# Optimization experiments

Measured on AMD Instinct MI355X. Metric: run time of the kernel, lower is better.

Reference implementation:

```python
import jax, jax.numpy as jnp
from jax import lax
import numpy as np

# Constants matching module config
DT = 0.0005            # integrator dt (phys_model default)
SPF = 10               # simulation substeps per output frame
GRAVITY = jnp.array([0.0, 0.0, -9.81], dtype=jnp.float32)
MASS_EPS = 0.1         # keep masses strictly positive

# ---- quaternion helpers (xyzw, matching warp layout: transform = [pos(3), quat(4)]) ----

def quat_mul(a, b):
    ax, ay, az, aw = a[..., 0], a[..., 1], a[..., 2], a[..., 3]
    bx, by, bz, bw = b[..., 0], b[..., 1], b[..., 2], b[..., 3]
    return jnp.stack([
        aw * bx + ax * bw + ay * bz - az * by,
        aw * by - ax * bz + ay * bw + az * bx,
        aw * bz + ax * by - ay * bx + az * bw,
        aw * bw - ax * bx - ay * by - az * bz,
    ], -1)


def quat_rotate(q, v):
    qv, qw = q[..., :3], q[..., 3:4]
    t = 2.0 * jnp.cross(qv, v)
    return v + qw * t + jnp.cross(qv, t)


def quat_from_axis_angle(axis, theta):
    # axis: (3,), theta: (bs,) -> (bs,4)
    half = 0.5 * theta
    return jnp.concatenate([axis[None, :] * jnp.sin(half)[:, None],
                            jnp.cos(half)[:, None]], -1)


def normalize(v, axis=-1):
    return v / jnp.linalg.norm(v, axis=axis, keepdims=True).clip(1e-8)


# ---- forward kinematics along the articulated chain (eval_fk) ----

def eval_fk(root_p, root_q, root_w, root_v, jq, jqd, axes, offsets):
    """root_*: (bs,...); jq,jqd: (bs,B); axes,offsets: (B,3).
    Returns body_q (bs,B+1,7), body_qd (bs,B+1,6) [angular,linear]."""
    def step(carry, inp):
        p, q, w, v = carry
        theta, thetad, axis, off = inp
        off_w = quat_rotate(q, off)                   # (bs,3)
        p_c = p + off_w
        q_c = quat_mul(q, quat_from_axis_angle(axis, theta))
        axis_w = quat_rotate(q, axis)
        w_c = w + axis_w * thetad[:, None]
        v_c = v + jnp.cross(w, off_w)
        carry = (p_c, q_c, w_c, v_c)
        return carry, carry
    inps = (jq.T, jqd.T, axes, offsets)               # leading dim B
    _, (ps, qs, ws, vs) = lax.scan(step, (root_p, root_q, root_w, root_v), inps)
    body_p = jnp.concatenate([root_p[None], ps], 0)   # (B+1,bs,3)
    body_r = jnp.concatenate([root_q[None], qs], 0)
    body_w = jnp.concatenate([root_w[None], ws], 0)
    body_v = jnp.concatenate([root_v[None], vs], 0)
    body_q = jnp.concatenate([body_p, body_r], -1).transpose(1, 0, 2)   # (bs,B+1,7)
    body_qd = jnp.concatenate([body_w, body_v], -1).transpose(1, 0, 2)  # (bs,B+1,6)
    return body_q, body_qd


def reference(q_init, qd_init, torques, res_f, refs, target_ke, target_kd,
              body_mass, joint_axes, joint_offsets):
    bs, ndof = q_init.shape
    B = ndof - 7
    axes = normalize(joint_axes)                      # (B,3)
    mass = body_mass + MASS_EPS                       # (bs,B+1)

    # initial maximal-coordinate state from generalized coords
    root_p = q_init[:, 0:3]
    root_q = normalize(q_init[:, 3:7])
    root_w = qd_init[:, 0:3]
    root_v = qd_init[:, 3:6]
    jq = q_init[:, 7:]
    jqd = qd_init[:, 6:]

    def sim_step(state, u):
        p, q, w, v, jq, jqd = state
        tau, ref, rf = u                              # (bs,6+B),(bs,6+B),(bs,B+1,6)
        m0 = mass[:, 0:1]
        # free root body: residual wrench + act wrench + gravity, semi-implicit Euler
        v = v + DT * ((tau[:, 3:6] + rf[:, 0, 3:6]) / m0 + GRAVITY)
        w = w + DT * (tau[:, 0:3] + rf[:, 0, 0:3]) / m0
        p = p + DT * v
        wq = jnp.concatenate([w, jnp.zeros_like(w[:, :1])], -1)
        q = normalize(q + DT * 0.5 * quat_mul(wq, q))
        # revolute joints: PD target (ke,kd) + actuation + residual torque on axis
        rf_tau = jnp.einsum('nbd,bd->nb', rf[:, 1:, 0:3], axes)   # (bs,B)
        tau_j = tau[:, 6:] + target_ke * (ref[:, 6:] - jq) - target_kd * jqd + rf_tau
        jqd = jqd + DT * tau_j / mass[:, 1:]
        jq = jq + DT * jqd
        return (p, q, w, v, jq, jqd), None

    def frame_step(state, u_frame):
        state, _ = lax.scan(sim_step, state, u_frame)
        p, q, w, v, jq, jqd = state
        bq, bqd = eval_fk(p, q, w, v, jq, jqd, axes, joint_offsets)
        return state, (bq, bqd)

    nsteps = torques.shape[0]
    F = nsteps // SPF                                 # output frames after frame 0
    u = (torques.reshape(F, SPF, bs, -1),
         refs.reshape(F, SPF, bs, -1),
         res_f.reshape(F, SPF, bs, B + 1, 6))

    state0 = (root_p, root_q, root_w, root_v, jq, jqd)
    bq0, bqd0 = eval_fk(*state0, axes, joint_offsets)  # frame 0 = init FK
    _, (bqs, bqds) = lax.scan(frame_step, state0, u)
    wp_pos = jnp.concatenate([bq0[None], bqs], 0)      # (T,bs,B+1,7)
    wp_vel = jnp.concatenate([bqd0[None], bqds], 0)    # (T,bs,B+1,6)
    return wp_pos, wp_vel


def setup_inputs() -> dict:
    key = jax.random.key(0)
    ks = jax.random.split(key, 10)
    bs, B, S = 1024, 25, 150
    return {
        'q_init': jax.random.normal(ks[0], (bs, 7 + B), jnp.float32),
        'qd_init': 0.1 * jax.random.normal(ks[1], (bs, 6 + B), jnp.float32),
        'torques': jax.random.normal(ks[2], (S, bs, 6 + B), jnp.float32),
        'res_f': jax.random.normal(ks[3], (S, bs, B + 1, 6), jnp.float32),
        'refs': jax.random.normal(ks[4], (S, bs, 6 + B), jnp.float32),
        'target_ke': jax.random.uniform(ks[5], (bs, B), jnp.float32),
        'target_kd': jax.random.uniform(ks[6], (bs, B), jnp.float32),
        'body_mass': jax.random.uniform(ks[7], (bs, B + 1), jnp.float32),
        'joint_axes': jax.random.normal(ks[8], (B, 3), jnp.float32),
        'joint_offsets': 0.2 * jax.random.normal(ks[9], (B, 3), jnp.float32),
    }
```

## Files before the change

### kernel.cpp

```cpp
#include <hip/hip_runtime.h>

#define DT     0.0005f
#define NENV   1024
#define NB     25
#define SPF    10
#define NFRM   16
#define SNAP_STRIDE 64

#define JTHREADS (NENV*NB)
#define JBLOCKS  (JTHREADS/64)
#define RBLOCKS  (NENV/64)
#define TQ_SLAB  (NENV*31)
#define RF_SLAB  (NENV*156)

__global__ __launch_bounds__(64) void integrate_kernel(
    const float* __restrict__ q_init,
    const float* __restrict__ qd_init,
    const float* __restrict__ torques,
    const float* __restrict__ res_f,
    const float* __restrict__ refs,
    const float* __restrict__ target_ke,
    const float* __restrict__ target_kd,
    const float* __restrict__ body_mass,
    const float* __restrict__ joint_axes,
    float* __restrict__ snap)
{
    const int bid = (int)blockIdx.x;

    if (bid < JBLOCKS) {
        const int t   = bid*64 + (int)threadIdx.x;
        const int env = t / NB;
        const int j   = t - env*NB;

        float a0 = joint_axes[j*3+0];
        float a1 = joint_axes[j*3+1];
        float a2 = joint_axes[j*3+2];
        float rn = 1.0f / fmaxf(sqrtf(a0*a0 + a1*a1 + a2*a2), 1e-8f);
        const float ax = a0*rn, ay = a1*rn, az = a2*rn;
        const float ke   = target_ke[env*NB + j];
        const float kd   = target_kd[env*NB + j];
        const float invm = 1.0f / (body_mass[env*(NB+1) + 1 + j] + 0.1f);
        float jq  = q_init [env*32 + 7 + j];
        float jqd = qd_init[env*31 + 6 + j];

        const int tq_off = env*31  + 6 + j;
        const int rf_off = env*156 + 6 + 6*j;

        snap[(size_t)env*SNAP_STRIDE + 13 + j] = jq;
        snap[(size_t)env*SNAP_STRIDE + 38 + j] = jqd;

        #pragma unroll 1
        for (int f = 1; f < NFRM; ++f) {
            float ta[SPF], rr[SPF], r0[SPF], r1[SPF], r2[SPF];
            #pragma unroll
            for (int k = 0; k < SPF; ++k) {
                const int s = (f-1)*SPF + k;
                ta[k] = torques[(size_t)s*TQ_SLAB + tq_off];
                rr[k] = refs   [(size_t)s*TQ_SLAB + tq_off];
                const float* rf = res_f + (size_t)s*RF_SLAB + rf_off;
                float2 ab = *(const float2*)rf;
                r0[k] = ab.x; r1[k] = ab.y; r2[k] = rf[2];
            }
            #pragma unroll
            for (int k = 0; k < SPF; ++k) {
                float rftau = r0[k]*ax + r1[k]*ay + r2[k]*az;
                float tj = ta[k] + ke*(rr[k] - jq) - kd*jqd + rftau;
                jqd += DT * tj * invm;
                jq  += DT * jqd;
            }
            float* sp = snap + ((size_t)f*NENV + env) * SNAP_STRIDE;
            sp[13 + j] = jq;
            sp[38 + j] = jqd;
        }
    } else {
        const int env = (bid - JBLOCKS)*64 + (int)threadIdx.x;

        float px = q_init[env*32+0], py = q_init[env*32+1], pz = q_init[env*32+2];
        float q0 = q_init[env*32+3], q1 = q_init[env*32+4];
        float q2 = q_init[env*32+5], q3 = q_init[env*32+6];
        float rn = 1.0f / fmaxf(sqrtf(q0*q0 + q1*q1 + q2*q2 + q3*q3), 1e-8f);
        float qx = q0*rn, qy = q1*rn, qz = q2*rn, qw = q3*rn;
        float wx = qd_init[env*31+0], wy = qd_init[env*31+1], wz = qd_init[env*31+2];
        float vx = qd_init[env*31+3], vy = qd_init[env*31+4], vz = qd_init[env*31+5];
        const float invm0 = 1.0f / (body_mass[env*(NB+1)] + 0.1f);

        {
            float* sp = snap + (size_t)env * SNAP_STRIDE;
            sp[0]=px; sp[1]=py; sp[2]=pz;
            sp[3]=qx; sp[4]=qy; sp[5]=qz; sp[6]=qw;
            sp[7]=wx; sp[8]=wy; sp[9]=wz;
            sp[10]=vx; sp[11]=vy; sp[12]=vz;
        }

        #pragma unroll 1
        for (int f = 1; f < NFRM; ++f) {
            float  tb[SPF][6];
            float4 ra[SPF];
            float2 rb[SPF];
            #pragma unroll
            for (int k = 0; k < SPF; ++k) {
                const int s = (f-1)*SPF + k;
                const float* tq = torques + (size_t)s*TQ_SLAB + env*31;
                tb[k][0]=tq[0]; tb[k][1]=tq[1]; tb[k][2]=tq[2];
                tb[k][3]=tq[3]; tb[k][4]=tq[4]; tb[k][5]=tq[5];
                const float* rf = res_f + (size_t)s*RF_SLAB + env*156;
                ra[k] = *(const float4*)rf;
                rb[k] = *(const float2*)(rf + 4);
            }
            #pragma unroll
            for (int k = 0; k < SPF; ++k) {
                vx += DT * ((tb[k][3] + rb[k].x) * invm0);
                vy += DT * ((tb[k][4] + rb[k].y) * invm0);
                vz += DT * ((tb[k][5] + ra[k].w) * invm0 - 9.81f);
                wx += DT * (tb[k][0] + ra[k].x) * invm0;
                wy += DT * (tb[k][1] + ra[k].y) * invm0;
                wz += DT * (tb[k][2] + ra[k].z) * invm0;
                px += DT * vx; py += DT * vy; pz += DT * vz;
                float dqx =  wx*qw + wy*qz - wz*qy;
                float dqy = -wx*qz + wy*qw + wz*qx;
                float dqz =  wx*qy - wy*qx + wz*qw;
                float dqw = -(wx*qx + wy*qy + wz*qz);
                float nqx = qx + 0.5f*DT*dqx;
                float nqy = qy + 0.5f*DT*dqy;
                float nqz = qz + 0.5f*DT*dqz;
                float nqw = qw + 0.5f*DT*dqw;
                float nrm = sqrtf(nqx*nqx + nqy*nqy + nqz*nqz + nqw*nqw);
                float rq  = 1.0f / fmaxf(nrm, 1e-8f);
                qx = nqx*rq; qy = nqy*rq; qz = nqz*rq; qw = nqw*rq;
            }
            float* sp = snap + ((size_t)f*NENV + env) * SNAP_STRIDE;
            sp[0]=px; sp[1]=py; sp[2]=pz;
            sp[3]=qx; sp[4]=qy; sp[5]=qz; sp[6]=qw;
            sp[7]=wx; sp[8]=wy; sp[9]=wz;
            sp[10]=vx; sp[11]=vy; sp[12]=vz;
        }
    }
}

__global__ __launch_bounds__(64) void integrate_kernel_fixed(
    const float* __restrict__ q_init,
    const float* __restrict__ qd_init,
    const float* __restrict__ torques,
    const float* __restrict__ res_f,
    const float* __restrict__ refs,
    const float* __restrict__ target_ke,
    const float* __restrict__ target_kd,
    const float* __restrict__ body_mass,
    const float* __restrict__ joint_axes,
    float* __restrict__ snap)
{
    const int bid = (int)blockIdx.x;

    if (bid < JBLOCKS) {
        const int t   = bid*64 + (int)threadIdx.x;
        const int env = t / NB;
        const int j   = t - env*NB;

        float a0 = joint_axes[j*3+0];
        float a1 = joint_axes[j*3+1];
        float a2 = joint_axes[j*3+2];
        float rn = 1.0f / fmaxf(sqrtf(a0*a0 + a1*a1 + a2*a2), 1e-8f);
        const float ax = a0*rn, ay = a1*rn, az = a2*rn;
        const float ke   = target_ke[env*NB + j];
        const float kd   = target_kd[env*NB + j];
        const float invm = 1.0f / (body_mass[env*(NB+1) + 1 + j] + 0.1f);
        float jq  = q_init [env*32 + 7 + j];
        float jqd = qd_init[env*31 + 6 + j];

        const int tq_off = env*31  + 6 + j;
        const int rf_off = env*156 + 6 + 6*j;

        snap[(size_t)env*SNAP_STRIDE + 13 + j] = jq;
        snap[(size_t)env*SNAP_STRIDE + 38 + j] = jqd;

        #pragma unroll 1
        for (int f = 1; f < NFRM; ++f) {
            float ta[SPF], rr[SPF], r0[SPF], r1[SPF], r2[SPF];
            #pragma unroll
            for (int k = 0; k < SPF; ++k) {
                const int s = (f-1)*SPF + k;
                ta[k] = torques[(size_t)s*TQ_SLAB + tq_off];
                rr[k] = refs   [(size_t)s*TQ_SLAB + tq_off];
                const float* rf = res_f + (size_t)s*RF_SLAB + rf_off;
                float2 ab = *(const float2*)rf;
                r0[k] = ab.x; r1[k] = ab.y; r2[k] = rf[2];
            }
            #pragma unroll
            for (int k = 0; k < SPF; ++k) {
                float rftau = r0[k]*ax + r1[k]*ay + r2[k]*az;
                float tj = ta[k] + ke*(rr[k] - jq) - kd*jqd + rftau;
                jqd += DT * tj * invm;
                jq  += DT * jqd;
            }
            float* sp = snap + ((size_t)f*NENV + env) * SNAP_STRIDE;
            sp[13 + j] = jq;
            sp[38 + j] = jqd;
        }
    } else {
        const int env = (bid - JBLOCKS)*64 + (int)threadIdx.x;

        float px = q_init[env*32+0], py = q_init[env*32+1], pz = q_init[env*32+2];
        float q0 = q_init[env*32+3], q1 = q_init[env*32+4];
        float q2 = q_init[env*32+5], q3 = q_init[env*32+6];
        float rn = 1.0f / fmaxf(sqrtf(q0*q0 + q1*q1 + q2*q2 + q3*q3), 1e-8f);
        float qx = q0*rn, qy = q1*rn, qz = q2*rn, qw = q3*rn;
        float wx = qd_init[env*31+0], wy = qd_init[env*31+1], wz = qd_init[env*31+2];
        float vx = qd_init[env*31+3], vy = qd_init[env*31+4], vz = qd_init[env*31+5];
        const float invm0 = 1.0f / (body_mass[env*(NB+1)] + 0.1f);

        {
            float* sp = snap + (size_t)env * SNAP_STRIDE;
            sp[0]=px; sp[1]=py; sp[2]=pz;
            sp[3]=qx; sp[4]=qy; sp[5]=qz; sp[6]=qw;
            sp[7]=wx; sp[8]=wy; sp[9]=wz;
            sp[10]=vx; sp[11]=vy; sp[12]=vz;
        }

        #pragma unroll 1
        for (int f = 1; f < NFRM; ++f) {
            float  tb[SPF][6];
            float4 ra[SPF];
            float2 rb[SPF];
            #pragma unroll
            for (int k = 0; k < SPF; ++k) {
                const int s = (f-1)*SPF + k;
                const float* tq = torques + (size_t)s*TQ_SLAB + env*31;
                tb[k][0]=tq[0]; tb[k][1]=tq[1]; tb[k][2]=tq[2];
                tb[k][3]=tq[3]; tb[k][4]=tq[4]; tb[k][5]=tq[5];
                const float* rf = res_f + (size_t)s*RF_SLAB + env*156;
                ra[k] = *(const float4*)rf;
                rb[k] = *(const float2*)(rf + 4);
            }
            #pragma unroll
            for (int k = 0; k < SPF; ++k) {
                vx += DT * ((tb[k][3] + ra[k].w) * invm0);
                vy += DT * ((tb[k][4] + rb[k].x) * invm0);
                vz += DT * ((tb[k][5] + rb[k].y) * invm0 - 9.81f);
                wx += DT * (tb[k][0] + ra[k].x) * invm0;
                wy += DT * (tb[k][1] + ra[k].y) * invm0;
                wz += DT * (tb[k][2] + ra[k].z) * invm0;
                px += DT * vx; py += DT * vy; pz += DT * vz;
                float dqx =  wx*qw + wy*qz - wz*qy;
                float dqy = -wx*qz + wy*qw + wz*qx;
                float dqz =  wx*qy - wy*qx + wz*qw;
                float dqw = -(wx*qx + wy*qy + wz*qz);
                float nqx = qx + 0.5f*DT*dqx;
                float nqy = qy + 0.5f*DT*dqy;
                float nqz = qz + 0.5f*DT*dqz;
                float nqw = qw + 0.5f*DT*dqw;
                float nrm = sqrtf(nqx*nqx + nqy*nqy + nqz*nqz + nqw*nqw);
                float rq  = 1.0f / fmaxf(nrm, 1e-8f);
                qx = nqx*rq; qy = nqy*rq; qz = nqz*rq; qw = nqw*rq;
            }
            float* sp = snap + ((size_t)f*NENV + env) * SNAP_STRIDE;
            sp[0]=px; sp[1]=py; sp[2]=pz;
            sp[3]=qx; sp[4]=qy; sp[5]=qz; sp[6]=qw;
            sp[7]=wx; sp[8]=wy; sp[9]=wz;
            sp[10]=vx; sp[11]=vy; sp[12]=vz;
        }
    }
}

__global__ __launch_bounds__(64) void fk_kernel(
    const float* __restrict__ snap,
    const float* __restrict__ joint_axes,
    const float* __restrict__ joint_offsets,
    float* __restrict__ out)
{
    const int t = (int)(blockIdx.x * blockDim.x + threadIdx.x);
    const int f = t >> 10;
    const int n = t & (NENV-1);

    float st[64];
    {
        const float4* sp4 = (const float4*)(snap + (size_t)t * SNAP_STRIDE);
        #pragma unroll
        for (int i = 0; i < 16; ++i) ((float4*)st)[i] = sp4[i];
    }

    float px=st[0], py=st[1], pz=st[2];
    float qx=st[3], qy=st[4], qz=st[5], qw=st[6];
    float wx=st[7], wy=st[8], wz=st[9];
    float vx=st[10], vy=st[11], vz=st[12];

    float* pos = out + ((size_t)f*NENV + n) * (26*7);
    float* vel = out + (size_t)NFRM*NENV*26*7 + ((size_t)f*NENV + n) * (26*6);

    pos[0]=px; pos[1]=py; pos[2]=pz; pos[3]=qx; pos[4]=qy; pos[5]=qz; pos[6]=qw;
    vel[0]=wx; vel[1]=wy; vel[2]=wz; vel[3]=vx; vel[4]=vy; vel[5]=vz;

    #pragma unroll
    for (int b = 0; b < NB; ++b) {
        float a0=joint_axes[b*3+0], a1=joint_axes[b*3+1], a2=joint_axes[b*3+2];
        float rn = 1.0f / fmaxf(sqrtf(a0*a0 + a1*a1 + a2*a2), 1e-8f);
        float axn=a0*rn, ayn=a1*rn, azn=a2*rn;
        float ox=joint_offsets[b*3+0], oy=joint_offsets[b*3+1], oz=joint_offsets[b*3+2];

        float tx = 2.0f*(qy*oz - qz*oy);
        float ty = 2.0f*(qz*ox - qx*oz);
        float tz = 2.0f*(qx*oy - qy*ox);
        float owx = ox + qw*tx + (qy*tz - qz*ty);
        float owy = oy + qw*ty + (qz*tx - qx*tz);
        float owz = oz + qw*tz + (qx*ty - qy*tx);

        float pcx = px + owx, pcy = py + owy, pcz = pz + owz;

        float half = 0.5f * st[13+b];
        float sh, ch;
        __sincosf(half, &sh, &ch);
        float bx = axn*sh, by = ayn*sh, bz = azn*sh, bw = ch;
        float qcx = qw*bx + qx*bw + qy*bz - qz*by;
        float qcy = qw*by - qx*bz + qy*bw + qz*bx;
        float qcz = qw*bz + qx*by - qy*bx + qz*bw;
        float qcw = qw*bw - qx*bx - qy*by - qz*bz;

        float ux = 2.0f*(qy*azn - qz*ayn);
        float uy = 2.0f*(qz*axn - qx*azn);
        float uz = 2.0f*(qx*ayn - qy*axn);
        float awx = axn + qw*ux + (qy*uz - qz*uy);
        float awy = ayn + qw*uy + (qz*ux - qx*uz);
        float awz = azn + qw*uz + (qx*uy - qy*ux);

        float thd = st[38+b];
        float wcx = wx + awx*thd, wcy = wy + awy*thd, wcz = wz + awz*thd;
        float vcx = vx + (wy*owz - wz*owy);
        float vcy = vy + (wz*owx - wx*owz);
        float vcz = vz + (wx*owy - wy*owx);

        px=pcx; py=pcy; pz=pcz;
        qx=qcx; qy=qcy; qz=qcz; qw=qcw;
        wx=wcx; wy=wcy; wz=wcz;
        vx=vcx; vy=vcy; vz=vcz;

        float* pb = pos + (size_t)(b+1)*7;
        pb[0]=px; pb[1]=py; pb[2]=pz; pb[3]=qx; pb[4]=qy; pb[5]=qz; pb[6]=qw;
        float* vb = vel + (size_t)(b+1)*6;
        vb[0]=wx; vb[1]=wy; vb[2]=wz; vb[3]=vx; vb[4]=vy; vb[5]=vz;
    }
}

extern "C" void kernel_launch(void* const* d_in, const int* in_sizes, int n_in,
                              void* d_out, int out_size, void* d_ws, size_t ws_size,
                              hipStream_t stream)
{
    const float* q_init     = (const float*)d_in[0];
    const float* qd_init    = (const float*)d_in[1];
    const float* torques    = (const float*)d_in[2];
    const float* res_f      = (const float*)d_in[3];
    const float* refs       = (const float*)d_in[4];
    const float* target_ke  = (const float*)d_in[5];
    const float* target_kd  = (const float*)d_in[6];
    const float* body_mass  = (const float*)d_in[7];
    const float* joint_axes = (const float*)d_in[8];
    const float* joint_offs = (const float*)d_in[9];
    float* out  = (float*)d_out;
    float* snap = (float*)d_ws;

    integrate_kernel_fixed<<<dim3(JBLOCKS + RBLOCKS), dim3(64), 0, stream>>>(
        q_init, qd_init, torques, res_f, refs,
        target_ke, target_kd, body_mass, joint_axes, snap);

    fk_kernel<<<dim3(NFRM*NENV/64), dim3(64), 0, stream>>>(
        snap, joint_axes, joint_offs, out);
}
```

Measured before the change: 267.5 us.

## Parallelize joint integration across frames via linear-recurrence scan and stage FK output in LDS

The per-joint integrator is linear in (q, qd), so each frame's 10 substeps are recast as an affine map. The forcing contribution for every frame is computed in parallel across frames by a new kernel, and a second kernel composes the maps sequentially. This removes the 15-frame serial dependency from the memory-heavy loop and raises parallelism. The FK kernel now stages per-thread outputs in shared memory and writes them back as coalesced float4 stores, in two passes for positions and velocities. The cost is an extra kernel launch, a workspace buffer, a fallback path and different float rounding from reassociating the recurrence.

Result: slower. 367.9 us (+37.5%).

```diff
diff --git a/kernel.cpp b/kernel.cpp
--- a/kernel.cpp
+++ b/kernel.cpp
@@ -5,15 +5,17 @@
 #define NB     25
 #define SPF    10
 #define NFRM   16
+#define NF01   15
+#define TQ_SLAB (NENV*31)
+#define RF_SLAB (NENV*156)
 #define SNAP_STRIDE 64
-
-#define JTHREADS (NENV*NB)
-#define JBLOCKS  (JTHREADS/64)
-#define RBLOCKS  (NENV/64)
-#define TQ_SLAB  (NENV*31)
-#define RF_SLAB  (NENV*156)
-
-__global__ __launch_bounds__(64) void integrate_kernel(
+#define SNAP_FLOATS (NFRM*NENV*SNAP_STRIDE)
+#define NJ      (NENV*NB)
+#define K1_JBLOCKS (NJ*NF01/256)
+#define K1_RBLOCKS (NENV/256)
+#define WS_NEED_BYTES ((size_t)(SNAP_FLOATS + NJ*NF01*2)*4)
+
+__global__ void k1_kernel(
     const float* __restrict__ q_init,
     const float* __restrict__ qd_init,
     const float* __restrict__ torques,
@@ -23,14 +25,16 @@
     const float* __restrict__ target_kd,
     const float* __restrict__ body_mass,
     const float* __restrict__ joint_axes,
-    float* __restrict__ snap)
+    float* __restrict__ snap,
+    float2* __restrict__ cws)
 {
     const int bid = (int)blockIdx.x;
-
-    if (bid < JBLOCKS) {
-        const int t   = bid*64 + (int)threadIdx.x;
-        const int env = t / NB;
-        const int j   = t - env*NB;
+    if (bid < K1_JBLOCKS) {
+        const int g   = bid*256 + (int)threadIdx.x;
+        const int f01 = g / NJ;
+        const int r   = g - f01*NJ;
+        const int env = r / NB;
+        const int j   = r - env*NB;
 
         float a0 = joint_axes[j*3+0];
         float a1 = joint_axes[j*3+1];
@@ -40,164 +44,34 @@
         const float ke   = target_ke[env*NB + j];
         const float kd   = target_kd[env*NB + j];
         const float invm = 1.0f / (body_mass[env*(NB+1) + 1 + j] + 0.1f);
-        float jq  = q_init [env*32 + 7 + j];
-        float jqd = qd_init[env*31 + 6 + j];
+        const float dti  = DT*invm;
+        const float a11  = 1.0f - DT*kd*invm;
+        const float a10  = -DT*ke*invm;
 
         const int tq_off = env*31  + 6 + j;
         const int rf_off = env*156 + 6 + 6*j;
 
-        snap[(size_t)env*SNAP_STRIDE + 13 + j] = jq;
-        snap[(size_t)env*SNAP_STRIDE + 38 + j] = jqd;
-
-        #pragma unroll 1
-        for (int f = 1; f < NFRM; ++f) {
-            float ta[SPF], rr[SPF], r0[SPF], r1[SPF], r2[SPF];
-            #pragma unroll
-            for (int k = 0; k < SPF; ++k) {
-                const int s = (f-1)*SPF + k;
-                ta[k] = torques[(size_t)s*TQ_SLAB + tq_off];
-                rr[k] = refs   [(size_t)s*TQ_SLAB + tq_off];
-                const float* rf = res_f + (size_t)s*RF_SLAB + rf_off;
-                float2 ab = *(const float2*)rf;
-                r0[k] = ab.x; r1[k] = ab.y; r2[k] = rf[2];
-            }
-            #pragma unroll
-            for (int k = 0; k < SPF; ++k) {
-                float rftau = r0[k]*ax + r1[k]*ay + r2[k]*az;
-                float tj = ta[k] + ke*(rr[k] - jq) - kd*jqd + rftau;
-                jqd += DT * tj * invm;
-                jq  += DT * jqd;
-            }
-            float* sp = snap + ((size_t)f*NENV + env) * SNAP_STRIDE;
-            sp[13 + j] = jq;
-            sp[38 + j] = jqd;
-        }
+        float  ta[SPF], rr[SPF], r2[SPF];
+        float2 ab[SPF];
+        #pragma unroll
+        for (int k = 0; k < SPF; ++k) {
+            const int s = f01*SPF + k;
+            ta[k] = torques[(size_t)s*TQ_SLAB + tq_off];
+            rr[k] = refs   [(size_t)s*TQ_SLAB + tq_off];
+            const float* rf = res_f + (size_t)s*RF_SLAB + rf_off;
+            ab[k] = *(const float2*)rf;
+            r2[k] = rf[2];
+        }
+        float cq = 0.0f, cd = 0.0f;
+        #pragma unroll
+        for (int k = 0; k < SPF; ++k) {
+            float u = ta[k] + ke*rr[k] + (ab[k].x*ax + ab[k].y*ay + r2[k]*az);
+            cd = a10*cq + a11*cd + dti*u;
+            cq += DT*cd;
+        }
+        cws[(size_t)f01*NJ + r] = make_float2(cq, cd);
     } else {
-        const int env = (bid - JBLOCKS)*64 + (int)threadIdx.x;
-
-        float px = q_init[env*32+0], py = q_init[env*32+1], pz = q_init[env*32+2];
-        float q0 = q_init[env*32+3], q1 = q_init[env*32+4];
-        float q2 = q_init[env*32+5], q3 = q_init[env*32+6];
-        float rn = 1.0f / fmaxf(sqrtf(q0*q0 + q1*q1 + q2*q2 + q3*q3), 1e-8f);
-        float qx = q0*rn, qy = q1*rn, qz = q2*rn, qw = q3*rn;
-        float wx = qd_init[env*31+0], wy = qd_init[env*31+1], wz = qd_init[env*31+2];
-        float vx = qd_init[env*31+3], vy = qd_init[env*31+4], vz = qd_init[env*31+5];
-        const float invm0 = 1.0f / (body_mass[env*(NB+1)] + 0.1f);
-
-        {
-            float* sp = snap + (size_t)env * SNAP_STRIDE;
-            sp[0]=px; sp[1]=py; sp[2]=pz;
-            sp[3]=qx; sp[4]=qy; sp[5]=qz; sp[6]=qw;
-            sp[7]=wx; sp[8]=wy; sp[9]=wz;
-            sp[10]=vx; sp[11]=vy; sp[12]=vz;
-        }
-
-        #pragma unroll 1
-        for (int f = 1; f < NFRM; ++f) {
-            float  tb[SPF][6];
-            float4 ra[SPF];
-            float2 rb[SPF];
-            #pragma unroll
-            for (int k = 0; k < SPF; ++k) {
-                const int s = (f-1)*SPF + k;
-                const float* tq = torques + (size_t)s*TQ_SLAB + env*31;
-                tb[k][0]=tq[0]; tb[k][1]=tq[1]; tb[k][2]=tq[2];
-                tb[k][3]=tq[3]; tb[k][4]=tq[4]; tb[k][5]=tq[5];
-                const float* rf = res_f + (size_t)s*RF_SLAB + env*156;
-                ra[k] = *(const float4*)rf;
-                rb[k] = *(const float2*)(rf + 4);
-            }
-            #pragma unroll
-            for (int k = 0; k < SPF; ++k) {
-                vx += DT * ((tb[k][3] + rb[k].x) * invm0);
-                vy += DT * ((tb[k][4] + rb[k].y) * invm0);
-                vz += DT * ((tb[k][5] + ra[k].w) * invm0 - 9.81f);
-                wx += DT * (tb[k][0] + ra[k].x) * invm0;
-                wy += DT * (tb[k][1] + ra[k].y) * invm0;
-                wz += DT * (tb[k][2] + ra[k].z) * invm0;
-                px += DT * vx; py += DT * vy; pz += DT * vz;
-                float dqx =  wx*qw + wy*qz - wz*qy;
-                float dqy = -wx*qz + wy*qw + wz*qx;
-                float dqz =  wx*qy - wy*qx + wz*qw;
-                float dqw = -(wx*qx + wy*qy + wz*qz);
-                float nqx = qx + 0.5f*DT*dqx;
-                float nqy = qy + 0.5f*DT*dqy;
-                float nqz = qz + 0.5f*DT*dqz;
-                float nqw = qw + 0.5f*DT*dqw;
-                float nrm = sqrtf(nqx*nqx + nqy*nqy + nqz*nqz + nqw*nqw);
-                float rq  = 1.0f / fmaxf(nrm, 1e-8f);
-                qx = nqx*rq; qy = nqy*rq; qz = nqz*rq; qw = nqw*rq;
-            }
-            float* sp = snap + ((size_t)f*NENV + env) * SNAP_STRIDE;
-            sp[0]=px; sp[1]=py; sp[2]=pz;
-            sp[3]=qx; sp[4]=qy; sp[5]=qz; sp[6]=qw;
-            sp[7]=wx; sp[8]=wy; sp[9]=wz;
-            sp[10]=vx; sp[11]=vy; sp[12]=vz;
-        }
-    }
-}
-
-__global__ __launch_bounds__(64) void integrate_kernel_fixed(
-    const float* __restrict__ q_init,
-    const float* __restrict__ qd_init,
-    const float* __restrict__ torques,
-    const float* __restrict__ res_f,
-    const float* __restrict__ refs,
-    const float* __restrict__ target_ke,
-    const float* __restrict__ target_kd,
-    const float* __restrict__ body_mass,
-    const float* __restrict__ joint_axes,
-    float* __restrict__ snap)
-{
-    const int bid = (int)blockIdx.x;
-
-    if (bid < JBLOCKS) {
-        const int t   = bid*64 + (int)threadIdx.x;
-        const int env = t / NB;
-        const int j   = t - env*NB;
-
-        float a0 = joint_axes[j*3+0];
-        float a1 = joint_axes[j*3+1];
-        float a2 = joint_axes[j*3+2];
-        float rn = 1.0f / fmaxf(sqrtf(a0*a0 + a1*a1 + a2*a2), 1e-8f);
-        const float ax = a0*rn, ay = a1*rn, az = a2*rn;
-        const float ke   = target_ke[env*NB + j];
-        const float kd   = target_kd[env*NB + j];
-        const float invm = 1.0f / (body_mass[env*(NB+1) + 1 + j] + 0.1f);
-        float jq  = q_init [env*32 + 7 + j];
-        float jqd = qd_init[env*31 + 6 + j];
-
-        const int tq_off = env*31  + 6 + j;
-        const int rf_off = env*156 + 6 + 6*j;
-
-        snap[(size_t)env*SNAP_STRIDE + 13 + j] = jq;
-        snap[(size_t)env*SNAP_STRIDE + 38 + j] = jqd;
-
-        #pragma unroll 1
-        for (int f = 1; f < NFRM; ++f) {
-            float ta[SPF], rr[SPF], r0[SPF], r1[SPF], r2[SPF];
-            #pragma unroll
-            for (int k = 0; k < SPF; ++k) {
-                const int s = (f-1)*SPF + k;
-                ta[k] = torques[(size_t)s*TQ_SLAB + tq_off];
-                rr[k] = refs   [(size_t)s*TQ_SLAB + tq_off];
-                const float* rf = res_f + (size_t)s*RF_SLAB + rf_off;
-                float2 ab = *(const float2*)rf;
-                r0[k] = ab.x; r1[k] = ab.y; r2[k] = rf[2];
-            }
-            #pragma unroll
-            for (int k = 0; k < SPF; ++k) {
-                float rftau = r0[k]*ax + r1[k]*ay + r2[k]*az;
-                float tj = ta[k] + ke*(rr[k] - jq) - kd*jqd + rftau;
-                jqd += DT * tj * invm;
-                jq  += DT * jqd;
-            }
-            float* sp = snap + ((size_t)f*NENV + env) * SNAP_STRIDE;
-            sp[13 + j] = jq;
-            sp[38 + j] = jqd;
-        }
-    } else {
-        const int env = (bid - JBLOCKS)*64 + (int)threadIdx.x;
+        const int env = (bid - K1_JBLOCKS)*256 + (int)threadIdx.x;
 
         float px = q_init[env*32+0], py = q_init[env*32+1], pz = q_init[env*32+2];
         float q0 = q_init[env*32+3], q1 = q_init[env*32+4];
@@ -261,33 +135,72 @@
     }
 }
 
-__global__ __launch_bounds__(64) void fk_kernel(
-    const float* __restrict__ snap,
+__global__ void k2_kernel(
+    const float* __restrict__ q_init,
+    const float* __restrict__ qd_init,
+    const float* __restrict__ target_ke,
+    const float* __restrict__ target_kd,
+    const float* __restrict__ body_mass,
+    const float2* __restrict__ cws,
+    float* __restrict__ snap)
+{
+    const int r   = (int)(blockIdx.x*256 + threadIdx.x);
+    const int env = r / NB;
+    const int j   = r - env*NB;
+
+    const float ke   = target_ke[env*NB + j];
+    const float kd   = target_kd[env*NB + j];
+    const float invm = 1.0f / (body_mass[env*(NB+1) + 1 + j] + 0.1f);
+    const float a11  = 1.0f - DT*kd*invm;
+    const float a10  = -DT*ke*invm;
+
+    float m00 = 1.0f, m10 = 0.0f, m01 = 0.0f, m11 = 1.0f;
+    #pragma unroll
+    for (int k = 0; k < SPF; ++k) {
+        m10 = a10*m00 + a11*m10;  m00 += DT*m10;
+        m11 = a10*m01 + a11*m11;  m01 += DT*m11;
+    }
+
+    float jq  = q_init [env*32 + 7 + j];
+    float jqd = qd_init[env*31 + 6 + j];
+
+    snap[(size_t)env*SNAP_STRIDE + 13 + j] = jq;
+    snap[(size_t)env*SNAP_STRIDE + 38 + j] = jqd;
+
+    float2 c[NF01];
+    #pragma unroll
+    for (int f = 0; f < NF01; ++f) c[f] = cws[(size_t)f*NJ + r];
+
+    #pragma unroll
+    for (int f = 0; f < NF01; ++f) {
+        float nq = m00*jq + m01*jqd + c[f].x;
+        float nd = m10*jq + m11*jqd + c[f].y;
+        jq = nq; jqd = nd;
+        float* sp = snap + ((size_t)(f+1)*NENV + env) * SNAP_STRIDE;
+        sp[13 + j] = jq;
+        sp[38 + j] = jqd;
+    }
+}
+
+template<int PASS>
+__device__ __forceinline__ void fk_chain(
+    const float st[64],
     const float* __restrict__ joint_axes,
     const float* __restrict__ joint_offsets,
-    float* __restrict__ out)
-{
-    const int t = (int)(blockIdx.x * blockDim.x + threadIdx.x);
-    const int f = t >> 10;
-    const int n = t & (NENV-1);
-
-    float st[64];
-    {
-        const float4* sp4 = (const float4*)(snap + (size_t)t * SNAP_STRIDE);
-        #pragma unroll
-        for (int i = 0; i < 16; ++i) ((float4*)st)[i] = sp4[i];
-    }
-
+    float* __restrict__ lds, int tid)
+{
     float px=st[0], py=st[1], pz=st[2];
     float qx=st[3], qy=st[4], qz=st[5], qw=st[6];
     float wx=st[7], wy=st[8], wz=st[9];
     float vx=st[10], vy=st[11], vz=st[12];
 
-    float* pos = out + ((size_t)f*NENV + n) * (26*7);
-    float* vel = out + (size_t)NFRM*NENV*26*7 + ((size_t)f*NENV + n) * (26*6);
-
-    pos[0]=px; pos[1]=py; pos[2]=pz; pos[3]=qx; pos[4]=qy; pos[5]=qz; pos[6]=qw;
-    vel[0]=wx; vel[1]=wy; vel[2]=wz; vel[3]=vx; vel[4]=vy; vel[5]=vz;
+    if (PASS == 0) {
+        float* p = lds + tid*182;
+        p[0]=px; p[1]=py; p[2]=pz; p[3]=qx; p[4]=qy; p[5]=qz; p[6]=qw;
+    } else {
+        float* p = lds + tid*156;
+        p[0]=wx; p[1]=wy; p[2]=wz; p[3]=vx; p[4]=vy; p[5]=vz;
+    }
 
     #pragma unroll
     for (int b = 0; b < NB; ++b) {
@@ -332,10 +245,153 @@
         wx=wcx; wy=wcy; wz=wcz;
         vx=vcx; vy=vcy; vz=vcz;
 
-        float* pb = pos + (size_t)(b+1)*7;
-        pb[0]=px; pb[1]=py; pb[2]=pz; pb[3]=qx; pb[4]=qy; pb[5]=qz; pb[6]=qw;
-        float* vb = vel + (size_t)(b+1)*6;
-        vb[0]=wx; vb[1]=wy; vb[2]=wz; vb[3]=vx; vb[4]=vy; vb[5]=vz;
+        if (PASS == 0) {
+            float* p = lds + tid*182 + (b+1)*7;
+            p[0]=px; p[1]=py; p[2]=pz; p[3]=qx; p[4]=qy; p[5]=qz; p[6]=qw;
+        } else {
+            float* p = lds + tid*156 + (b+1)*6;
+            p[0]=wx; p[1]=wy; p[2]=wz; p[3]=vx; p[4]=vy; p[5]=vz;
+        }
+    }
+}
+
+__global__ __launch_bounds__(64) void fk_kernel(
+    const float* __restrict__ snap,
+    const float* __restrict__ joint_axes,
+    const float* __restrict__ joint_offsets,
+    float* __restrict__ out)
+{
+    __shared__ float lds[64*182];
+    const int tid = (int)threadIdx.x;
+    const int t   = (int)blockIdx.x*64 + tid;
+    const int f   = t >> 10;
+    const int e0  = (int)((blockIdx.x*64) & 1023);
+
+    float st[64];
+    {
+        const float4* sp4 = (const float4*)(snap + (size_t)t * SNAP_STRIDE);
+        #pragma unroll
+        for (int i = 0; i < 16; ++i) ((float4*)st)[i] = sp4[i];
+    }
+
+    fk_chain<0>(st, joint_axes, joint_offsets, lds, tid);
+    __syncthreads();
+    {
+        float4* o4 = (float4*)(out + (size_t)(f*NENV + e0)*182);
+        const float4* l4 = (const float4*)lds;
+        for (int i = tid; i < 64*182/4; i += 64) o4[i] = l4[i];
+    }
+    __syncthreads();
+    fk_chain<1>(st, joint_axes, joint_offsets, lds, tid);
+    __syncthreads();
+    {
+        float4* o4 = (float4*)(out + (size_t)NFRM*NENV*182 + (size_t)(f*NENV + e0)*156);
+        const float4* l4 = (const float4*)lds;
+        for (int i = tid; i < 64*156/4; i += 64) o4[i] = l4[i];
+    }
+}
+
+__global__ __launch_bounds__(64) void integrate_fallback(
+    const float* __restrict__ q_init,
+    const float* __restrict__ qd_init,
+    const float* __restrict__ torques,
+    const float* __restrict__ res_f,
+    const float* __restrict__ refs,
+    const float* __restrict__ target_ke,
+    const float* __restrict__ target_kd,
+    const float* __restrict__ body_mass,
+    const float* __restrict__ joint_axes,
+    float* __restrict__ snap)
+{
+    const int bid = (int)blockIdx.x;
+    if (bid < NJ/64) {
+        const int t   = bid*64 + (int)threadIdx.x;
+        const int env = t / NB;
+        const int j   = t - env*NB;
+        float a0 = joint_axes[j*3+0], a1 = joint_axes[j*3+1], a2 = joint_axes[j*3+2];
+        float rn = 1.0f / fmaxf(sqrtf(a0*a0 + a1*a1 + a2*a2), 1e-8f);
+        const float ax = a0*rn, ay = a1*rn, az = a2*rn;
+        const float ke   = target_ke[env*NB + j];
+        const float kd   = target_kd[env*NB + j];
+        const float invm = 1.0f / (body_mass[env*(NB+1) + 1 + j] + 0.1f);
+        float jq  = q_init [env*32 + 7 + j];
+        float jqd = qd_init[env*31 + 6 + j];
+        const int tq_off = env*31  + 6 + j;
+        const int rf_off = env*156 + 6 + 6*j;
+        snap[(size_t)env*SNAP_STRIDE + 13 + j] = jq;
+        snap[(size_t)env*SNAP_STRIDE + 38 + j] = jqd;
+        #pragma unroll 1
+        for (int f = 1; f < NFRM; ++f) {
+            float ta[SPF], rr[SPF], r0[SPF], r1[SPF], r2[SPF];
+            #pragma unroll
+            for (int k = 0; k < SPF; ++k) {
+                const int s = (f-1)*SPF + k;
+                ta[k] = torques[(size_t)s*TQ_SLAB + tq_off];
+                rr[k] = refs   [(size_t)s*TQ_SLAB + tq_off];
+                const float* rf = res_f + (size_t)s*RF_SLAB + rf_off;
+                float2 ab = *(const float2*)rf;
+                r0[k] = ab.x; r1[k] = ab.y; r2[k] = rf[2];
+            }
+            #pragma unroll
+            for (int k = 0; k < SPF; ++k) {
+                float rftau = r0[k]*ax + r1[k]*ay + r2[k]*az;
+                float tj = ta[k] + ke*(rr[k] - jq) - kd*jqd + rftau;
+                jqd += DT * tj * invm;
+                jq  += DT * jqd;
+            }
+            float* sp = snap + ((size_t)f*NENV + env) * SNAP_STRIDE;
+            sp[13 + j] = jq; sp[38 + j] = jqd;
+        }
+    } else {
+        const int env = (bid - NJ/64)*64 + (int)threadIdx.x;
+        float px = q_init[env*32+0], py = q_init[env*32+1], pz = q_init[env*32+2];
+        float q0 = q_init[env*32+3], q1 = q_init[env*32+4];
+        float q2 = q_init[env*32+5], q3 = q_init[env*32+6];
+        float rn = 1.0f / fmaxf(sqrtf(q0*q0 + q1*q1 + q2*q2 + q3*q3), 1e-8f);
+        float qx = q0*rn, qy = q1*rn, qz = q2*rn, qw = q3*rn;
+        float wx = qd_init[env*31+0], wy = qd_init[env*31+1], wz = qd_init[env*31+2];
+        float vx = qd_init[env*31+3], vy = qd_init[env*31+4], vz = qd_init[env*31+5];
+        const float invm0 = 1.0f / (body_mass[env*(NB+1)] + 0.1f);
+        {
+            float* sp = snap + (size_t)env * SNAP_STRIDE;
+            sp[0]=px; sp[1]=py; sp[2]=pz; sp[3]=qx; sp[4]=qy; sp[5]=qz; sp[6]=qw;
+            sp[7]=wx; sp[8]=wy; sp[9]=wz; sp[10]=vx; sp[11]=vy; sp[12]=vz;
+        }
+        #pragma unroll 1
+        for (int f = 1; f < NFRM; ++f) {
+            float  tb[SPF][6]; float4 ra[SPF]; float2 rb[SPF];
+            #pragma unroll
+            for (int k = 0; k < SPF; ++k) {
+                const int s = (f-1)*SPF + k;
+                const float* tq = torques + (size_t)s*TQ_SLAB + env*31;
+                tb[k][0]=tq[0]; tb[k][1]=tq[1]; tb[k][2]=tq[2];
+                tb[k][3]=tq[3]; tb[k][4]=tq[4]; tb[k][5]=tq[5];
+                const float* rf = res_f + (size_t)s*RF_SLAB + env*156;
+                ra[k] = *(const float4*)rf; rb[k] = *(const float2*)(rf + 4);
+            }
+            #pragma unroll
+            for (int k = 0; k < SPF; ++k) {
+                vx += DT * ((tb[k][3] + ra[k].w) * invm0);
+                vy += DT * ((tb[k][4] + rb[k].x) * invm0);
+                vz += DT * ((tb[k][5] + rb[k].y) * invm0 - 9.81f);
+                wx += DT * (tb[k][0] + ra[k].x) * invm0;
+                wy += DT * (tb[k][1] + ra[k].y) * invm0;
+                wz += DT * (tb[k][2] + ra[k].z) * invm0;
+                px += DT * vx; py += DT * vy; pz += DT * vz;
+                float dqx =  wx*qw + wy*qz - wz*qy;
+                float dqy = -wx*qz + wy*qw + wz*qx;
+                float dqz =  wx*qy - wy*qx + wz*qw;
+                float dqw = -(wx*qx + wy*qy + wz*qz);
+                float nqx = qx + 0.5f*DT*dqx, nqy = qy + 0.5f*DT*dqy;
+                float nqz = qz + 0.5f*DT*dqz, nqw = qw + 0.5f*DT*dqw;
+                float nrm = sqrtf(nqx*nqx + nqy*nqy + nqz*nqz + nqw*nqw);
+                float rq  = 1.0f / fmaxf(nrm, 1e-8f);
+                qx = nqx*rq; qy = nqy*rq; qz = nqz*rq; qw = nqw*rq;
+            }
+            float* sp = snap + ((size_t)f*NENV + env) * SNAP_STRIDE;
+            sp[0]=px; sp[1]=py; sp[2]=pz; sp[3]=qx; sp[4]=qy; sp[5]=qz; sp[6]=qw;
+            sp[7]=wx; sp[8]=wy; sp[9]=wz; sp[10]=vx; sp[11]=vy; sp[12]=vz;
+        }
     }
 }
 
@@ -353,12 +409,21 @@
     const float* body_mass  = (const float*)d_in[7];
     const float* joint_axes = (const float*)d_in[8];
     const float* joint_offs = (const float*)d_in[9];
-    float* out  = (float*)d_out;
-    float* snap = (float*)d_ws;
-
-    integrate_kernel_fixed<<<dim3(JBLOCKS + RBLOCKS), dim3(64), 0, stream>>>(
-        q_init, qd_init, torques, res_f, refs,
-        target_ke, target_kd, body_mass, joint_axes, snap);
+    float*  out  = (float*)d_out;
+    float*  snap = (float*)d_ws;
+    float2* cws  = (float2*)((float*)d_ws + SNAP_FLOATS);
+
+    if (ws_size >= WS_NEED_BYTES) {
+        k1_kernel<<<dim3(K1_JBLOCKS + K1_RBLOCKS), dim3(256), 0, stream>>>(
+            q_init, qd_init, torques, res_f, refs,
+            target_ke, target_kd, body_mass, joint_axes, snap, cws);
+        k2_kernel<<<dim3(NJ/256), dim3(256), 0, stream>>>(
+            q_init, qd_init, target_ke, target_kd, body_mass, cws, snap);
+    } else {
+        integrate_fallback<<<dim3(NJ/64 + NENV/64), dim3(64), 0, stream>>>(
+            q_init, qd_init, torques, res_f, refs,
+            target_ke, target_kd, body_mass, joint_axes, snap);
+    }
 
     fk_kernel<<<dim3(NFRM*NENV/64), dim3(64), 0, stream>>>(
         snap, joint_axes, joint_offs, out);
```
